# Kernel optimization log

Measured on AMD Instinct MI355X. Metric: run time of the kernel, lower is better.

Reference implementation:

```python
import jax, jax.numpy as jnp
import numpy as np

EPS = 1e-6
OMEGA = 0.1


def setup_inputs() -> dict:
    key = jax.random.key(0)
    k1, k2 = jax.random.split(key)
    n, d, kk = 4096, 128, 4
    inputs = jax.random.uniform(k1, (n, d), dtype=jnp.float32)  # positive so log(sim) is finite
    labels = jax.random.randint(k2, (n, kk), 0, 64, dtype=jnp.int64)
    return {"inputs": inputs, "labels": labels}


def reference(inputs, labels):
    n, kk = labels.shape
    sim = inputs @ inputs.T                      # [n, n]
    logsim = jnp.log(sim + EPS)                  # a_{jk} = log(sim[j,k]+eps)
    targets = labels[:, 0]
    eye = jnp.eye(n, dtype=bool)
    # pos_mask[j,k] = (targets[j] == targets[k]) xor diagonal
    pos = (targets[:, None] == targets[None, :]) & ~eye
    # eq[j,l,i] = (labels[l,i] == targets[j])
    eq = targets[:, None, None] == labels[None, :, :]
    m_idx = jnp.arange(kk)
    cols = kk - 1 - m_idx                        # neg_mask[m] uses label column kk-1-m
    # neg_mask[m][j,l] == 1  <=>  ~eq[j,l,kk-1-m]  AND  (m==0 or eq[j,l,kk-m])
    neq_col = ~eq[:, :, cols]                    # [j,l,m]
    prev_ok = jnp.concatenate(
        [jnp.ones((n, n, 1), dtype=bool), eq[:, :, cols[:-1]]], axis=-1)
    neg = neq_col & prev_ok                      # [j,l,m]
    # loss_pair[m] = log(Omega+eps) - log(Omega^(kk-m+1)+eps)
    lp = jnp.log(OMEGA + EPS) - jnp.log(OMEGA ** (kk - m_idx + 1) + EPS)  # [kk]
    dt = logsim.dtype
    posf = pos.astype(dt)
    negf = neg.astype(dt)
    # term = (a_jk - b_jlm)^2 with b_jlm = logsim[j,l] + 0.1*lp[m]
    # expand: sum_jklm pos*neg*(a^2 - 2ab + b^2), separable over k and (l,m)
    c = posf.sum(1)                              # [j] count of positives
    S1 = (posf * logsim).sum(1)                  # [j] sum a
    S2 = (posf * logsim ** 2).sum(1)             # [j] sum a^2
    b = logsim[:, :, None] + 0.1 * lp[None, None, :]   # [j,l,m]
    Ncnt = negf.sum(1)                           # [j,m]
    T1 = (negf * b).sum(1)                       # [j,m]
    T2 = (negf * b ** 2).sum(1)                  # [j,m]
    loss = (S2[:, None] * Ncnt - 2.0 * S1[:, None] * T1 + c[:, None] * T2).sum()
    return loss
```

## Files before the change

kernel.cpp:

```cpp
#include <hip/hip_runtime.h>
#include <math.h>

constexpr int N = 4096;
constexpr int D = 128;

constexpr size_t XBF_OFF = 0;
constexpr size_t TAB_OFF = (size_t)1 << 20;
constexpr size_t ACC_OFF = TAB_OFF + 64 * 4096;
constexpr size_t LSD_OFF = ACC_OFF + 5 * N * 4;
constexpr size_t SUM_OFF = LSD_OFF + N * 4;

typedef __attribute__((ext_vector_type(8))) short short8;
typedef __attribute__((ext_vector_type(4))) float floatx4;
typedef __attribute__((address_space(1))) unsigned int gu32;
typedef __attribute__((address_space(3))) unsigned int lu32;

__device__ inline unsigned f2bf(float f) {
  unsigned u = __builtin_bit_cast(unsigned, f);
  return (u + 0x7FFFu + ((u >> 16) & 1u)) >> 16;
}

__global__ __launch_bounds__(256) void k1_prep(
    const float* __restrict__ X, const int* __restrict__ labels,
    char* __restrict__ ws, float* __restrict__ out,
    float B0, float B1, float B2, float B3,
    float Q0, float Q1, float Q2, float Q3) {
  const int b = blockIdx.x, tid = threadIdx.x;
  if (b < 64) {
    const int t = b;
    __shared__ float red[4][4];
    unsigned char* tabu8 = (unsigned char*)(ws + TAB_OFF) + (size_t)t * N;
    float sg0 = 0.f, sgB = 0.f, sgQ = 0.f, ce0 = 0.f;
#pragma unroll 4
    for (int k = 0; k < 16; ++k) {
      const int j = k * 256 + tid;
      const int4 L = ((const int4*)labels)[j];
      const bool e0 = (t == L.x), e1 = (t == L.y), e2 = (t == L.z), e3 = (t == L.w);
      const bool n1 = e3 && !e2, n2 = e2 && !e1, n3 = e1 && !e0;
      sg0 += (e3 ? 0.f : 1.f) + (n1 ? 1.f : 0.f) + (n2 ? 1.f : 0.f) + (n3 ? 1.f : 0.f);
      sgB += (e3 ? 0.f : B0) + (n1 ? B1 : 0.f) + (n2 ? B2 : 0.f) + (n3 ? B3 : 0.f);
      sgQ += (e3 ? 0.f : Q0) + (n1 ? Q1 : 0.f) + (n2 ? Q2 : 0.f) + (n3 ? Q3 : 0.f);
      ce0 += e0 ? 1.f : 0.f;
      tabu8[j] = (unsigned char)((e1 ? 1u : 0u) | (e2 ? 2u : 0u) | (e3 ? 4u : 0u) | (e0 ? 8u : 0u));
    }
    const int w = tid >> 6, lane = tid & 63;
#pragma unroll
    for (int s = 1; s <= 32; s <<= 1) {
      sg0 += __shfl_xor(sg0, s, 64); sgB += __shfl_xor(sgB, s, 64);
      sgQ += __shfl_xor(sgQ, s, 64); ce0 += __shfl_xor(ce0, s, 64);
    }
    if (lane == 0) { red[w][0] = sg0; red[w][1] = sgB; red[w][2] = sgQ; red[w][3] = ce0; }
    __syncthreads();
    if (tid == 0) {
      float* sums = (float*)(ws + SUM_OFF);
      sums[t * 4 + 0] = red[0][0] + red[1][0] + red[2][0] + red[3][0];
      sums[t * 4 + 1] = red[0][1] + red[1][1] + red[2][1] + red[3][1];
      sums[t * 4 + 2] = red[0][2] + red[1][2] + red[2][2] + red[3][2];
      sums[t * 4 + 3] = red[0][3] + red[1][3] + red[2][3] + red[3][3];
    }
  } else if (b < 320) {
    const int task = (b - 64) * 256 + tid;
    const int r   = task >> 4;
    const int blk = task & 15;
    const float4 x0 = *(const float4*)&X[r * D + blk * 8];
    const float4 x1 = *(const float4*)&X[r * D + blk * 8 + 4];
    uint4 wv;
    wv.x = f2bf(x0.x) | (f2bf(x0.y) << 16);
    wv.y = f2bf(x0.z) | (f2bf(x0.w) << 16);
    wv.z = f2bf(x1.x) | (f2bf(x1.y) << 16);
    wv.w = f2bf(x1.z) | (f2bf(x1.w) << 16);
    *(uint4*)(ws + XBF_OFF + (size_t)r * 256 + ((blk ^ (r & 15)) * 16)) = wv;
  } else if (b < 336) {
    const int i = (b - 320) * 256 + tid;
    const float* xr = X + i * D;
    float s = 0.f;
#pragma unroll
    for (int c = 0; c < 32; ++c) {
      const float4 v = ((const float4*)xr)[c];
      s += v.x * v.x + v.y * v.y + v.z * v.z + v.w * v.w;
    }
    ((float*)(ws + LSD_OFF))[i] = __logf(s + 1e-6f);
  } else {
    const int idx = (b - 336) * 256 + tid;
    ((float*)(ws + ACC_OFF))[idx] = 0.f;
    if (idx == 0) out[0] = 0.f;
  }
}

__global__ __launch_bounds__(512, 4) void logratio_phaseA(
    const char* __restrict__ ws_ro, const int* __restrict__ labels,
    float* acc5, float B0, float B1, float B2, float B3) {

  __shared__ __align__(16) char smem[65792];

  const int tid  = threadIdx.x;
  const int w    = tid >> 6;
  const int lane = tid & 63;
  const int lc   = lane & 15;
  const int quad = lane >> 4;
  const int jBase = blockIdx.x * 128;
  const int iBase = blockIdx.y * 128;

  float4* pal = (float4*)(smem + 65536);
  if (tid < 16) {
    const bool e1 = tid & 1, e2 = tid & 2, e3 = tid & 4, e0 = tid & 8;
    const bool n1 = e3 && !e2, n2 = e2 && !e1, n3 = e1 && !e0;
    const float g0 = (e3 ? 0.f : 1.f) + (n1 ? 1.f : 0.f) + (n2 ? 1.f : 0.f) + (n3 ? 1.f : 0.f);
    const float gB = (e3 ? 0.f : B0) + (n1 ? B1 : 0.f) + (n2 ? B2 : 0.f) + (n3 ? B3 : 0.f);
    pal[tid] = make_float4(gB, g0, e0 ? 1.f : 0.f, 0.f);
  }

  const char* xbf = ws_ro + XBF_OFF;
  const char* gB_ = xbf + (size_t)jBase * 256 + w * 4096 + lane * 16;
  const char* gA_ = xbf + (size_t)iBase * 256 + w * 4096 + lane * 16;
#pragma unroll
  for (int c = 0; c < 4; ++c) {
    __builtin_amdgcn_global_load_lds((const gu32*)(gB_ + c * 1024),
                                     (lu32*)(smem + w * 4096 + c * 1024), 16, 0, 0);
    __builtin_amdgcn_global_load_lds((const gu32*)(gA_ + c * 1024),
                                     (lu32*)(smem + 32768 + w * 4096 + c * 1024), 16, 0, 0);
  }

  int tis[4];
#pragma unroll
  for (int reg = 0; reg < 4; ++reg)
    tis[reg] = labels[(iBase + w * 16 + quad * 4 + reg) * 4];

  __syncthreads();

  floatx4 acc[8] = {};
  const char* Abase = smem + 32768 + (w * 16 + lc) * 256;
#pragma unroll
  for (int kb = 0; kb < 4; ++kb) {
    const int pb = ((kb * 4 + quad) ^ lc) * 16;
    const short8 af = *(const short8*)(Abase + pb);
    short8 bfr[8];
#pragma unroll
    for (int tn = 0; tn < 8; ++tn)
      bfr[tn] = *(const short8*)(smem + (tn * 16 + lc) * 256 + pb);
#pragma unroll
    for (int tn = 0; tn < 8; ++tn)
      acc[tn] = __builtin_amdgcn_mfma_f32_16x16x32_bf16(af, bfr[tn], acc[tn], 0, 0, 0);
  }

  __syncthreads();
  float* Red = (float*)smem;

  const unsigned char* tabu8 = (const unsigned char*)(ws_ro + TAB_OFF);
#pragma unroll
  for (int reg = 0; reg < 4; ++reg) {
    const int row = w * 16 + quad * 4 + reg;
    const unsigned char* trow = tabu8 + (size_t)tis[reg] * N + jBase + lc;

    float U = 0.f, W = 0.f, V = 0.f, P1 = 0.f, P2 = 0.f;
#pragma unroll
    for (int tn = 0; tn < 8; ++tn) {
      const unsigned pat = trow[tn * 16];
      const float4 pe = pal[pat];
      const float ls = __logf(acc[tn][reg] + 1e-6f);
      const float u = pe.y * ls;
      U += u;
      W = fmaf(u, ls, W);
      V = fmaf(pe.x, ls, V);
      const float p = pe.z * ls;
      P1 += p;
      P2 = fmaf(p, ls, P2);
    }
    float* dst = Red + row * 81 + lc * 5;
    dst[0] = U; dst[1] = W; dst[2] = V; dst[3] = P1; dst[4] = P2;
  }
  __syncthreads();

  if (tid < 128) {
    const int gi = iBase + tid;
    const float* src = Red + tid * 81;
    float s0 = 0.f, s1 = 0.f, s2 = 0.f, s3 = 0.f, s4 = 0.f;
#pragma unroll
    for (int l = 0; l < 16; ++l) {
      s0 += src[l * 5 + 0]; s1 += src[l * 5 + 1]; s2 += src[l * 5 + 2];
      s3 += src[l * 5 + 3]; s4 += src[l * 5 + 4];
    }
    atomicAdd(&acc5[0 * N + gi], s0);
    atomicAdd(&acc5[1 * N + gi], s1);
    atomicAdd(&acc5[2 * N + gi], s2);
    atomicAdd(&acc5[3 * N + gi], s3);
    atomicAdd(&acc5[4 * N + gi], s4);
  }
}

__global__ __launch_bounds__(256) void logratio_phaseB(
    const char* __restrict__ ws_ro, const int* __restrict__ labels,
    float* out) {
  const int i = blockIdx.x * 256 + threadIdx.x;
  const float* acc5 = (const float*)(ws_ro + ACC_OFF);
  const float U  = acc5[0 * N + i];
  const float W  = acc5[1 * N + i];
  const float V  = acc5[2 * N + i];
  const float P1 = acc5[3 * N + i];
  const float P2 = acc5[4 * N + i];
  const int t = labels[i * 4];
  const float4 S = ((const float4*)(ws_ro + SUM_OFF))[t];
  const float lsd = ((const float*)(ws_ro + LSD_OFF))[i];
  const float c  = S.w - 1.f;
  const float S1 = P1 - lsd;
  const float S2 = P2 - lsd * lsd;
  const float A  = S.x;
  const float Bv = U + S.y;
  const float Cv = W + 2.f * V + S.z;
  float v = S2 * A - 2.f * S1 * Bv + c * Cv;
#pragma unroll
  for (int m = 32; m >= 1; m >>= 1) v += __shfl_xor(v, m, 64);
  __shared__ float wsum[4];
  if ((threadIdx.x & 63) == 0) wsum[threadIdx.x >> 6] = v;
  __syncthreads();
  if (threadIdx.x == 0) atomicAdd(out, wsum[0] + wsum[1] + wsum[2] + wsum[3]);
}

extern "C" void kernel_launch(void* const* d_in, const int* in_sizes, int n_in,
                              void* d_out, int out_size, void* d_ws, size_t ws_size,
                              hipStream_t stream) {
  const float* inputs = (const float*)d_in[0];
  const int* labels = (const int*)d_in[1];
  float* out = (float*)d_out;
  char* ws = (char*)d_ws;

  float Bq[4], Qq[4];
  for (int m = 0; m < 4; ++m) {
    const float lpv = logf(0.1f + 1e-6f) - logf(powf(0.1f, (float)(5 - m)) + 1e-6f);
    Bq[m] = 0.1f * lpv;
    Qq[m] = Bq[m] * Bq[m];
  }

  k1_prep<<<416, 256, 0, stream>>>(inputs, labels, ws, out,
                                   Bq[0], Bq[1], Bq[2], Bq[3],
                                   Qq[0], Qq[1], Qq[2], Qq[3]);
  dim3 grid(N / 128, N / 128);
  logratio_phaseA<<<grid, 512, 0, stream>>>(ws, labels, (float*)(ws + ACC_OFF),
                                            Bq[0], Bq[1], Bq[2], Bq[3]);
  logratio_phaseB<<<N / 256, 256, 0, stream>>>(ws, labels, out);
}
```

Measured before the change: 79.73 us.

## Exploit Gram matrix symmetry by computing only upper-triangular tile pairs

Replaces the full 32x32 tile grid with 528 upper-triangular tile blocks, mapping the linear block index to (bi, bj) by solving a quadratic. Each off-diagonal tile now also accumulates the column-side statistics, using the transposed pattern lookup, a cross-quad shuffle reduction and a second shared-memory buffer. This roughly halves the MFMA and log work and the tile loads. In exchange it adds extra table lookups, shuffles and atomics per off-diagonal block, plus more register pressure.

Result: slower. 125.7 us (+57.6%).

```diff
diff --git a/kernel.cpp b/kernel.cpp
--- a/kernel.cpp
+++ b/kernel.cpp
@@ -91,15 +91,20 @@
     const char* __restrict__ ws_ro, const int* __restrict__ labels,
     float* acc5, float B0, float B1, float B2, float B3) {
 
+  int k = blockIdx.x;
+  int bi = (int)((65.0 - sqrt(4225.0 - 8.0 * (double)k)) * 0.5);
+  while (bi > 0 && k < bi * 32 - bi * (bi - 1) / 2) --bi;
+  while (k >= (bi + 1) * 32 - (bi + 1) * bi / 2) ++bi;
+  const int bj = bi + (k - (bi * 32 - bi * (bi - 1) / 2));
+  const int iBase = bi * 128, jBase = bj * 128;
+  const bool offdiag = (bi != bj);
+
   __shared__ __align__(16) char smem[65792];
-
   const int tid  = threadIdx.x;
   const int w    = tid >> 6;
   const int lane = tid & 63;
   const int lc   = lane & 15;
   const int quad = lane >> 4;
-  const int jBase = blockIdx.x * 128;
-  const int iBase = blockIdx.y * 128;
 
   float4* pal = (float4*)(smem + 65536);
   if (tid < 16) {
@@ -121,10 +126,13 @@
                                      (lu32*)(smem + 32768 + w * 4096 + c * 1024), 16, 0, 0);
   }
 
-  int tis[4];
+  int tis[4], tcs[8];
 #pragma unroll
   for (int reg = 0; reg < 4; ++reg)
     tis[reg] = labels[(iBase + w * 16 + quad * 4 + reg) * 4];
+#pragma unroll
+  for (int tn = 0; tn < 8; ++tn)
+    tcs[tn] = labels[(jBase + tn * 16 + lc) * 4];
 
   __syncthreads();
 
@@ -144,30 +152,62 @@
   }
 
   __syncthreads();
-  float* Red = (float*)smem;
+  float* Red  = (float*)smem;
+  float* Red2 = (float*)(smem + 41472);
 
   const unsigned char* tabu8 = (const unsigned char*)(ws_ro + TAB_OFF);
+  const unsigned char* trow[4];
+#pragma unroll
+  for (int reg = 0; reg < 4; ++reg)
+    trow[reg] = tabu8 + (size_t)tis[reg] * N + jBase + lc;
+
+  float rU[4] = {}, rW[4] = {}, rV[4] = {}, rP1[4] = {}, rP2[4] = {};
+
+#pragma unroll
+  for (int tn = 0; tn < 8; ++tn) {
+    const unsigned char* tcol = tabu8 + (size_t)tcs[tn] * N + iBase + w * 16 + quad * 4;
+    float cU = 0.f, cW = 0.f, cV = 0.f, cP1 = 0.f, cP2 = 0.f;
+#pragma unroll
+    for (int reg = 0; reg < 4; ++reg) {
+      const float ls = __logf(acc[tn][reg] + 1e-6f);
+      {
+        const float4 pe = pal[trow[reg][tn * 16]];
+        const float u = pe.y * ls;
+        rU[reg] += u;
+        rW[reg] = fmaf(u, ls, rW[reg]);
+        rV[reg] = fmaf(pe.x, ls, rV[reg]);
+        const float p = pe.z * ls;
+        rP1[reg] += p;
+        rP2[reg] = fmaf(p, ls, rP2[reg]);
+      }
+      if (offdiag) {
+        const float4 pe = pal[tcol[reg]];
+        const float u = pe.y * ls;
+        cU += u;
+        cW = fmaf(u, ls, cW);
+        cV = fmaf(pe.x, ls, cV);
+        const float p = pe.z * ls;
+        cP1 += p;
+        cP2 = fmaf(p, ls, cP2);
+      }
+    }
+    if (offdiag) {
+#pragma unroll
+      for (int s = 16; s <= 32; s <<= 1) {
+        cU += __shfl_xor(cU, s, 64);  cW += __shfl_xor(cW, s, 64);
+        cV += __shfl_xor(cV, s, 64);  cP1 += __shfl_xor(cP1, s, 64);
+        cP2 += __shfl_xor(cP2, s, 64);
+      }
+      if (quad == 0) {
+        float* d2 = Red2 + (tn * 16 + lc) * 41 + w * 5;
+        d2[0] = cU; d2[1] = cW; d2[2] = cV; d2[3] = cP1; d2[4] = cP2;
+      }
+    }
+  }
 #pragma unroll
   for (int reg = 0; reg < 4; ++reg) {
-    const int row = w * 16 + quad * 4 + reg;
-    const unsigned char* trow = tabu8 + (size_t)tis[reg] * N + jBase + lc;
-
-    float U = 0.f, W = 0.f, V = 0.f, P1 = 0.f, P2 = 0.f;
-#pragma unroll
-    for (int tn = 0; tn < 8; ++tn) {
-      const unsigned pat = trow[tn * 16];
-      const float4 pe = pal[pat];
-      const float ls = __logf(acc[tn][reg] + 1e-6f);
-      const float u = pe.y * ls;
-      U += u;
-      W = fmaf(u, ls, W);
-      V = fmaf(pe.x, ls, V);
-      const float p = pe.z * ls;
-      P1 += p;
-      P2 = fmaf(p, ls, P2);
-    }
-    float* dst = Red + row * 81 + lc * 5;
-    dst[0] = U; dst[1] = W; dst[2] = V; dst[3] = P1; dst[4] = P2;
+    float* dst = Red + (w * 16 + quad * 4 + reg) * 81 + lc * 5;
+    dst[0] = rU[reg]; dst[1] = rW[reg]; dst[2] = rV[reg]; dst[3] = rP1[reg]; dst[4] = rP2[reg];
   }
   __syncthreads();
 
@@ -185,6 +225,21 @@
     atomicAdd(&acc5[2 * N + gi], s2);
     atomicAdd(&acc5[3 * N + gi], s3);
     atomicAdd(&acc5[4 * N + gi], s4);
+  } else if (tid < 256 && offdiag) {
+    const int col = tid - 128;
+    const int gj = jBase + col;
+    const float* src = Red2 + col * 41;
+    float s0 = 0.f, s1 = 0.f, s2 = 0.f, s3 = 0.f, s4 = 0.f;
+#pragma unroll
+    for (int l = 0; l < 8; ++l) {
+      s0 += src[l * 5 + 0]; s1 += src[l * 5 + 1]; s2 += src[l * 5 + 2];
+      s3 += src[l * 5 + 3]; s4 += src[l * 5 + 4];
+    }
+    atomicAdd(&acc5[0 * N + gj], s0);
+    atomicAdd(&acc5[1 * N + gj], s1);
+    atomicAdd(&acc5[2 * N + gj], s2);
+    atomicAdd(&acc5[3 * N + gj], s3);
+    atomicAdd(&acc5[4 * N + gj], s4);
   }
 }
 
@@ -234,8 +289,7 @@
   k1_prep<<<416, 256, 0, stream>>>(inputs, labels, ws, out,
                                    Bq[0], Bq[1], Bq[2], Bq[3],
                                    Qq[0], Qq[1], Qq[2], Qq[3]);
-  dim3 grid(N / 128, N / 128);
-  logratio_phaseA<<<grid, 512, 0, stream>>>(ws, labels, (float*)(ws + ACC_OFF),
-                                            Bq[0], Bq[1], Bq[2], Bq[3]);
+  logratio_phaseA<<<528, 512, 0, stream>>>(ws, labels, (float*)(ws + ACC_OFF),
+                                           Bq[0], Bq[1], Bq[2], Bq[3]);
   logratio_phaseB<<<N / 256, 256, 0, stream>>>(ws, labels, out);
 }
```

## Loop each phaseA block over four j-tiles with overlapped B-tile prefetch

Applied to the files above, without the earlier changes.

Each phaseA block now handles four consecutive 128-column j-tiles instead of one, so the grid shrinks from 32x32 to 8x32. The A tile is loaded once and reused across the four j-tiles, and the next B tile is prefetched into LDS while the log/palette epilogue of the current tile runs. Per-row partial sums stay in registers across tiles, which cuts the LDS reduction and global atomics to a quarter. The cost is fewer blocks (256), which may leave CUs underfilled on a large GPU, plus extra register pressure and more serialized work per block.

New measurement: 92.45 us. 1.16x slower.

```diff
diff --git a/kernel.cpp b/kernel.cpp
--- a/kernel.cpp
+++ b/kernel.cpp
@@ -98,8 +98,8 @@
   const int lane = tid & 63;
   const int lc   = lane & 15;
   const int quad = lane >> 4;
-  const int jBase = blockIdx.x * 128;
   const int iBase = blockIdx.y * 128;
+  const int jt0   = blockIdx.x * 4;
 
   float4* pal = (float4*)(smem + 65536);
   if (tid < 16) {
@@ -111,63 +111,83 @@
   }
 
   const char* xbf = ws_ro + XBF_OFF;
-  const char* gB_ = xbf + (size_t)jBase * 256 + w * 4096 + lane * 16;
-  const char* gA_ = xbf + (size_t)iBase * 256 + w * 4096 + lane * 16;
-#pragma unroll
-  for (int c = 0; c < 4; ++c) {
-    __builtin_amdgcn_global_load_lds((const gu32*)(gB_ + c * 1024),
+  {
+    const char* gA_ = xbf + (size_t)iBase * 256 + w * 4096 + lane * 16;
+#pragma unroll
+    for (int c = 0; c < 4; ++c)
+      __builtin_amdgcn_global_load_lds((const gu32*)(gA_ + c * 1024),
+                                       (lu32*)(smem + 32768 + w * 4096 + c * 1024), 16, 0, 0);
+  }
+  const char* gBband = xbf + (size_t)jt0 * 128 * 256 + w * 4096 + lane * 16;
+#pragma unroll
+  for (int c = 0; c < 4; ++c)
+    __builtin_amdgcn_global_load_lds((const gu32*)(gBband + c * 1024),
                                      (lu32*)(smem + w * 4096 + c * 1024), 16, 0, 0);
-    __builtin_amdgcn_global_load_lds((const gu32*)(gA_ + c * 1024),
-                                     (lu32*)(smem + 32768 + w * 4096 + c * 1024), 16, 0, 0);
-  }
 
   int tis[4];
 #pragma unroll
   for (int reg = 0; reg < 4; ++reg)
     tis[reg] = labels[(iBase + w * 16 + quad * 4 + reg) * 4];
-
-  __syncthreads();
-
-  floatx4 acc[8] = {};
+  const unsigned char* tabu8 = (const unsigned char*)(ws_ro + TAB_OFF);
+  const unsigned char* trow[4];
+#pragma unroll
+  for (int reg = 0; reg < 4; ++reg)
+    trow[reg] = tabu8 + (size_t)tis[reg] * N + lc;
+
+  float rU[4] = {}, rW[4] = {}, rV[4] = {}, rP1[4] = {}, rP2[4] = {};
+
   const char* Abase = smem + 32768 + (w * 16 + lc) * 256;
-#pragma unroll
-  for (int kb = 0; kb < 4; ++kb) {
-    const int pb = ((kb * 4 + quad) ^ lc) * 16;
-    const short8 af = *(const short8*)(Abase + pb);
-    short8 bfr[8];
-#pragma unroll
-    for (int tn = 0; tn < 8; ++tn)
-      bfr[tn] = *(const short8*)(smem + (tn * 16 + lc) * 256 + pb);
-#pragma unroll
-    for (int tn = 0; tn < 8; ++tn)
-      acc[tn] = __builtin_amdgcn_mfma_f32_16x16x32_bf16(af, bfr[tn], acc[tn], 0, 0, 0);
-  }
-
-  __syncthreads();
+#pragma unroll 1
+  for (int q = 0; q < 4; ++q) {
+    __syncthreads();
+
+    floatx4 acc[8] = {};
+#pragma unroll
+    for (int kb = 0; kb < 4; ++kb) {
+      const int pb = ((kb * 4 + quad) ^ lc) * 16;
+      const short8 af = *(const short8*)(Abase + pb);
+      short8 bfr[8];
+#pragma unroll
+      for (int tn = 0; tn < 8; ++tn)
+        bfr[tn] = *(const short8*)(smem + (tn * 16 + lc) * 256 + pb);
+#pragma unroll
+      for (int tn = 0; tn < 8; ++tn)
+        acc[tn] = __builtin_amdgcn_mfma_f32_16x16x32_bf16(af, bfr[tn], acc[tn], 0, 0, 0);
+    }
+    __syncthreads();
+
+    if (q < 3) {
+      const char* g = gBband + (size_t)(q + 1) * 32768;
+#pragma unroll
+      for (int c = 0; c < 4; ++c)
+        __builtin_amdgcn_global_load_lds((const gu32*)(g + c * 1024),
+                                         (lu32*)(smem + w * 4096 + c * 1024), 16, 0, 0);
+    }
+
+    const int jBase = (jt0 + q) * 128;
+#pragma unroll
+    for (int reg = 0; reg < 4; ++reg) {
+      const unsigned char* tr = trow[reg] + jBase;
+#pragma unroll
+      for (int tn = 0; tn < 8; ++tn) {
+        const float4 pe = pal[tr[tn * 16]];
+        const float ls = __logf(acc[tn][reg] + 1e-6f);
+        const float u = pe.y * ls;
+        rU[reg] += u;
+        rW[reg] = fmaf(u, ls, rW[reg]);
+        rV[reg] = fmaf(pe.x, ls, rV[reg]);
+        const float p = pe.z * ls;
+        rP1[reg] += p;
+        rP2[reg] = fmaf(p, ls, rP2[reg]);
+      }
+    }
+  }
+
   float* Red = (float*)smem;
-
-  const unsigned char* tabu8 = (const unsigned char*)(ws_ro + TAB_OFF);
 #pragma unroll
   for (int reg = 0; reg < 4; ++reg) {
-    const int row = w * 16 + quad * 4 + reg;
-    const unsigned char* trow = tabu8 + (size_t)tis[reg] * N + jBase + lc;
-
-    float U = 0.f, W = 0.f, V = 0.f, P1 = 0.f, P2 = 0.f;
-#pragma unroll
-    for (int tn = 0; tn < 8; ++tn) {
-      const unsigned pat = trow[tn * 16];
-      const float4 pe = pal[pat];
-      const float ls = __logf(acc[tn][reg] + 1e-6f);
-      const float u = pe.y * ls;
-      U += u;
-      W = fmaf(u, ls, W);
-      V = fmaf(pe.x, ls, V);
-      const float p = pe.z * ls;
-      P1 += p;
-      P2 = fmaf(p, ls, P2);
-    }
-    float* dst = Red + row * 81 + lc * 5;
-    dst[0] = U; dst[1] = W; dst[2] = V; dst[3] = P1; dst[4] = P2;
+    float* dst = Red + (w * 16 + quad * 4 + reg) * 81 + lc * 5;
+    dst[0] = rU[reg]; dst[1] = rW[reg]; dst[2] = rV[reg]; dst[3] = rP1[reg]; dst[4] = rP2[reg];
   }
   __syncthreads();
 
@@ -234,7 +254,7 @@
   k1_prep<<<416, 256, 0, stream>>>(inputs, labels, ws, out,
                                    Bq[0], Bq[1], Bq[2], Bq[3],
                                    Qq[0], Qq[1], Qq[2], Qq[3]);
-  dim3 grid(N / 128, N / 128);
+  dim3 grid(8, 32);
   logratio_phaseA<<<grid, 512, 0, stream>>>(ws, labels, (float*)(ws + ACC_OFF),
                                             Bq[0], Bq[1], Bq[2], Bq[3]);
   logratio_phaseB<<<N / 256, 256, 0, stream>>>(ws, labels, out);
```
